# Kernel tuning notes

Hardware: AMD Instinct MI355X
Metric: run time of the kernel (lower is better)

The kernel has to match this reference:

```python
import jax, jax.numpy as jnp
import numpy as np

B, N, M, D = 128, 256, 8, 768  # batch, input patches, memory tokens, embed dim


def setup_inputs() -> dict:
    key = jax.random.key(0)
    ks = jax.random.split(key, 6)
    w_scale = D ** -0.5
    return {
        "x": jax.random.normal(ks[0], (B, N, D), dtype=jnp.float32),
        "memory": jax.random.normal(ks[1], (M, D), dtype=jnp.float32) * 0.02,
        "Wq": jax.random.normal(ks[2], (D, D), dtype=jnp.float32) * w_scale,
        "bq": jnp.zeros((D,), dtype=jnp.float32),
        "Wk": jax.random.normal(ks[3], (D, D), dtype=jnp.float32) * w_scale,
        "bk": jnp.zeros((D,), dtype=jnp.float32),
        "Wv": jax.random.normal(ks[4], (D, D), dtype=jnp.float32) * w_scale,
        "bv": jnp.zeros((D,), dtype=jnp.float32),
        "Wo": jax.random.normal(ks[5], (D, D), dtype=jnp.float32) * w_scale,
        "bo": jnp.zeros((D,), dtype=jnp.float32),
    }


def reference(x, memory, Wq, bq, Wk, bk, Wv, bv, Wo, bo):
    b, n, d = x.shape
    m = memory.shape[0]
    t = n + m
    scaling = d ** -0.5  # mha.scaling = 1/sqrt(input_dim)
    # concat input patches with expanded memory tokens: [B, T, D]
    cat = jnp.concatenate([x, jnp.broadcast_to(memory[None], (b, m, d))], axis=1)
    q = cat @ Wq + bq
    k = cat @ Wk + bk
    v = cat @ Wv + bv
    # full attention matrix [B, T, T], softmax over keys
    att = jax.nn.softmax(jnp.einsum("bqd,bkd->bqk", q, k) * scaling, axis=-1)
    # post-softmax multiplicative mask: zero all rows for memory-token queries
    row_mask = (jnp.arange(t) < n).astype(att.dtype)[None, :, None]  # [1, T, 1]
    att = att * row_mask
    head_out = jnp.einsum("bqk,bkd->bqd", att, v)
    attended = head_out @ Wo + bo
    # return only the input-patch part (split(...)[0])
    return attended[:, :n, :]
```

## Files before the change

kernel.cpp:

```cpp
#include <hip/hip_runtime.h>
#include <hip/hip_bf16.h>

typedef __attribute__((ext_vector_type(4))) float f32x4;
typedef __attribute__((ext_vector_type(8))) short short8;
typedef __attribute__((ext_vector_type(4))) unsigned short us4;
typedef unsigned short u16;

#define DEVI __device__ __forceinline__

#define BB 128
#define NN 256
#define MMEM 8
#define DD 768
#define TT 264
#define TP 320
#define SP 384
#define AROWS2 33024

DEVI u16 f2bf(float f) {
  __hip_bfloat16 b = __float2bfloat16(f);
  u16 u; __builtin_memcpy(&u, &b, 2); return u;
}

DEVI void gload_lds16(const void* g, void* l) {
  __builtin_amdgcn_global_load_lds((const __attribute__((address_space(1))) void*)g,
                                   (__attribute__((address_space(3))) void*)l, 16, 0, 0);
}


__global__ __launch_bounds__(256)
void conv_x(const float* __restrict__ x, const float* __restrict__ mem, u16* __restrict__ Ab) {
  const long total4 = (long)AROWS2 * DD / 4;
  for (long i = (long)blockIdx.x * blockDim.x + threadIdx.x; i < total4;
       i += (long)gridDim.x * blockDim.x) {
    long e = i * 4;
    int row = (int)(e / DD);
    int cb  = (int)(e % DD);
    f32x4 v = {0.f, 0.f, 0.f, 0.f};
    if (row < BB * NN)             v = *(const f32x4*)(x   + (size_t)row * DD + cb);
    else if (row < BB * NN + MMEM) v = *(const f32x4*)(mem + (size_t)(row - BB * NN) * DD + cb);
    us4 o = {f2bf(v[0]), f2bf(v[1]), f2bf(v[2]), f2bf(v[3])};
    *(us4*)(Ab + e) = o;
  }
}

__global__ __launch_bounds__(256)
void conv_w(const float* __restrict__ Wq, const float* __restrict__ Wk,
            const float* __restrict__ Wv, const float* __restrict__ Wo,
            u16* __restrict__ Wqt, u16* __restrict__ Wkt,
            u16* __restrict__ Wvt, u16* __restrict__ Wot) {
  const int total = 4 * DD * DD;
  for (int i = blockIdx.x * blockDim.x + threadIdx.x; i < total;
       i += gridDim.x * blockDim.x) {
    int mat = i / (DD * DD), rem = i % (DD * DD);
    int j = rem / DD, d = rem % DD;
    const float* W = (mat == 0) ? Wq : (mat == 1) ? Wk : (mat == 2) ? Wv : Wo;
    u16* Wt = (mat == 0) ? Wqt : (mat == 1) ? Wkt : (mat == 2) ? Wvt : Wot;
    Wt[(size_t)j * DD + d] = f2bf(W[(size_t)d * DD + j]);
  }
}


#define BAR()    __builtin_amdgcn_s_barrier()
#define CFENCE() asm volatile("" ::: "memory")
#define VMW8()   asm volatile("s_waitcnt vmcnt(8)" ::: "memory")

#define STG(gb, isB, ss, rg, kt) do {                                          \
    const u16* _s = (gb) + (size_t)((rg) * 16 + srow) * DD + (kt) * 64 + scol; \
    char* _d = smem + (ss) * 65536 + (isB) * 32768 + (rg) * 2048;              \
    gload_lds16(_s, _d);                                                       \
    gload_lds16(_s + 32, _d + 1024);                                           \
  } while (0)

#define STG_A0(ss, kt) STG(Ab, 0, ss, ((w & 3) | ((w & 4) << 1)), kt)
#define STG_B0(ss, kt) STG(Bb, 1, ss, ((w & 1) | ((w & 6) << 1)), kt)
#define STG_A1(ss, kt) STG(Ab, 0, ss, (((w & 3) | ((w & 4) << 1)) + 4), kt)
#define STG_B1(ss, kt) STG(Bb, 1, ss, (((w & 1) | ((w & 6) << 1)) + 2), kt)

#define RD_A(dst, s, QM)                                                          \
  _Pragma("unroll") for (int mi = 0; mi < 4; ++mi)                                \
  _Pragma("unroll") for (int ks = 0; ks < 2; ++ks)                                \
    dst[mi][ks] = *(const short8*)(smem + (s) * 65536 +                           \
                    ((wm * 8 + (QM) * 4 + mi) * 2 + ks) * 1024 + fbase);

#define RD_B(dst, s, QN)                                                          \
  _Pragma("unroll") for (int ni = 0; ni < 2; ++ni)                                \
  _Pragma("unroll") for (int ks = 0; ks < 2; ++ks)                                \
    dst[ni][ks] = *(const short8*)(smem + (s) * 65536 + 32768 +                   \
                    ((wn * 4 + (QN) * 2 + ni) * 2 + ks) * 1024 + fbase);

#define MM(FA, FB, QM, QN)                                                        \
  _Pragma("unroll") for (int mi = 0; mi < 4; ++mi)                                \
  _Pragma("unroll") for (int ni = 0; ni < 2; ++ni)                                \
  _Pragma("unroll") for (int ks = 0; ks < 2; ++ks)                                \
    acc[(QM)*4+mi][(QN)*2+ni] = __builtin_amdgcn_mfma_f32_16x16x32_bf16(          \
        FA[mi][ks], FB[ni][ks], acc[(QM)*4+mi][(QN)*2+ni], 0, 0, 0);

template<int MODE>
__global__ __launch_bounds__(512)
void gemm256(const u16* __restrict__ A, const u16* __restrict__ Bq,
             const u16* __restrict__ Bk, const u16* __restrict__ Bv,
             const float* __restrict__ b0, const float* __restrict__ b1,
             const float* __restrict__ b2,
             u16* __restrict__ Oq, u16* __restrict__ Ok, u16* __restrict__ Ov,
             float* __restrict__ FO, int NT)
{
  extern __shared__ char smem[];
  const int tid = threadIdx.x;
  const int l = tid & 63;
  const int w = tid >> 6;
  const int wm = w >> 2, wn = w & 3;

  const int nwg = gridDim.x * gridDim.y;
  const int lin = blockIdx.y * gridDim.x + blockIdx.x;
  const int qq = nwg >> 3, rr = nwg & 7;
  const int xcd = lin & 7, idx = lin >> 3;
  const int wg = (xcd < rr ? xcd * (qq + 1) : rr * (qq + 1) + (xcd - rr) * qq) + idx;
  const int tn = wg % gridDim.x, tm = wg / gridDim.x;

  const u16* Ab = A + (size_t)tm * 256 * DD;
  const u16* Bb;
  int matsel = 0;
  if constexpr (MODE == 0) {
    matsel = tn / 3;
    const u16* Wp = (matsel == 0) ? Bq : (matsel == 1) ? Bk : Bv;
    Bb = Wp + (size_t)(tn % 3) * 256 * DD;
  } else {
    Bb = Bq + (size_t)tn * 256 * DD;
  }

  const int jj = (l < 32) ? l : (l ^ 2);
  const int srow = jj >> 2;
  const int scol = (jj & 3) * 8;
  const int fbase = (((l & 15) * 64) + ((l >> 4) * 16)) ^ (((l >> 3) & 1) << 5);

  f32x4 acc[8][4];
  #pragma unroll
  for (int i = 0; i < 8; ++i)
    #pragma unroll
    for (int jx = 0; jx < 4; ++jx) acc[i][jx] = (f32x4){0.f, 0.f, 0.f, 0.f};

  short8 fa0[4][2], fa1[4][2], fb0[2][2], fb1[2][2];

  STG_A0(0, 0); STG_B0(0, 0); STG_A1(0, 0); STG_B1(0, 0);

  for (int g = 0; g < NT; ++g) {
    const int s = g & 1, ss = s ^ 1;
    const int st = (g + 1 < NT) ? (g + 1) : 0;

    CFENCE(); BAR(); CFENCE();
    STG_A0(ss, st); STG_B0(ss, st); STG_A1(ss, st); STG_B1(ss, st);
    VMW8();
    BAR(); CFENCE();

    RD_A(fa0, s, 0); RD_B(fb0, s, 0);
    __builtin_amdgcn_s_setprio(1); MM(fa0, fb0, 0, 0); __builtin_amdgcn_s_setprio(0);
    RD_A(fa1, s, 1);
    __builtin_amdgcn_s_setprio(1); MM(fa1, fb0, 1, 0); __builtin_amdgcn_s_setprio(0);
    RD_B(fb1, s, 1);
    __builtin_amdgcn_s_setprio(1); MM(fa1, fb1, 1, 1); MM(fa0, fb1, 0, 1);
    __builtin_amdgcn_s_setprio(0);
  }

  const int fr = l & 15, fro = (l >> 4) * 4;
  if constexpr (MODE == 0) {
    const float* bias = (matsel == 0) ? b0 : (matsel == 1) ? b1 : b2;
    u16* ob = (matsel == 0) ? Oq : (matsel == 1) ? Ok : Ov;
    const int cb = (tn % 3) * 256 + wn * 64;
    const size_t rb = (size_t)tm * 256 + wm * 128;
    #pragma unroll
    for (int MI = 0; MI < 8; ++MI)
      #pragma unroll
      for (int NI = 0; NI < 4; ++NI) {
        const int col = cb + NI * 16 + fr;
        const float bvv = bias[col];
        #pragma unroll
        for (int r = 0; r < 4; ++r)
          ob[(rb + MI * 16 + fro + r) * DD + col] = f2bf(acc[MI][NI][r] + bvv);
      }
  } else {
    const int cb = tn * 256 + wn * 64;
    const size_t rb = (size_t)tm * 256 + wm * 128;
    #pragma unroll
    for (int MI = 0; MI < 8; ++MI)
      #pragma unroll
      for (int NI = 0; NI < 4; ++NI) {
        const int col = cb + NI * 16 + fr;
        const float bvv = b0[col];
        #pragma unroll
        for (int r = 0; r < 4; ++r)
          FO[(rb + MI * 16 + fro + r) * DD + col] = acc[MI][NI][r] + bvv;
      }
  }
}


template<int MODE>
__global__ __launch_bounds__(256)
void gemm_bt(const u16* __restrict__ A, const u16* __restrict__ Bm,
             const float* __restrict__ f0,
             u16* __restrict__ U0, float* __restrict__ F0, int Kdim)
{
  const int tid = threadIdx.x;
  const int l  = tid & 63;
  const int w  = tid >> 6;
  const int wm = w >> 1, wn = w & 1;
  const int tm = blockIdx.x, tn = blockIdx.y, z = blockIdx.z;

  __shared__ u16 lsA[128 * 32];
  __shared__ u16 lsB[128 * 32];

  const u16* Abase; int lda;
  if constexpr (MODE == 1)      { Abase = A + ((size_t)z * NN + tm * 128) * DD; lda = DD; }
  else                          { Abase = A + ((size_t)z * NN + tm * 128) * TP; lda = TP; }

  const u16* Bbase; int ldb;
  if constexpr (MODE == 1) { Bbase = Bm; ldb = DD; }
  else                     { Bbase = Bm + ((size_t)z * DD + tn * 128) * TP; ldb = TP; }

  f32x4 acc[4][4];
  #pragma unroll
  for (int i = 0; i < 4; i++)
    #pragma unroll
    for (int j = 0; j < 4; j++) acc[i][j] = (f32x4){0.f, 0.f, 0.f, 0.f};

  const int srow = l >> 2;
  const int scol = (l & 3) * 8;
  const int nkt = Kdim >> 5;

  for (int kt = 0; kt < nkt; ++kt) {
    const int kpos = kt * 32 + scol;
    #pragma unroll
    for (int q = 0; q < 2; ++q) {
      const int r = q * 64 + w * 16 + srow;
      gload_lds16(Abase + (size_t)r * lda + kpos, &lsA[q * 2048 + w * 512]);
    }
    #pragma unroll
    for (int q = 0; q < 2; ++q) {
      const int r = q * 64 + w * 16 + srow;
      const u16* src;
      if constexpr (MODE == 1) {
        const int t = tn * 128 + r;
        const int rr = (t < NN) ? (z * NN + t)
                     : ((t < TT) ? (BB * NN + t - NN) : BB * NN);
        src = Bm + (size_t)rr * DD + kpos;
      } else {
        src = Bbase + (size_t)r * ldb + kpos;
      }
      gload_lds16(src, &lsB[q * 2048 + w * 512]);
    }
    __syncthreads();

    const int fr = l & 15, fk = (l >> 4) * 8;
    short8 fa[4], fb[4];
    #pragma unroll
    for (int mi = 0; mi < 4; mi++)
      fa[mi] = *(const short8*)&lsA[(wm * 64 + mi * 16 + fr) * 32 + fk];
    #pragma unroll
    for (int ni = 0; ni < 4; ni++)
      fb[ni] = *(const short8*)&lsB[(wn * 64 + ni * 16 + fr) * 32 + fk];
    #pragma unroll
    for (int mi = 0; mi < 4; mi++)
      #pragma unroll
      for (int ni = 0; ni < 4; ni++)
        acc[mi][ni] = __builtin_amdgcn_mfma_f32_16x16x32_bf16(fa[mi], fb[ni], acc[mi][ni], 0, 0, 0);
    __syncthreads();
  }

  const int fr  = l & 15;
  const int fro = (l >> 4) * 4;

  if constexpr (MODE == 1) {
    const float scl = 0.03608439182435161f;
    float* Sb = F0 + (size_t)z * NN * SP;
    const int cb = tn * 128 + wn * 64;
    const int rb = tm * 128 + wm * 64;
    #pragma unroll
    for (int mi = 0; mi < 4; mi++)
      #pragma unroll
      for (int ni = 0; ni < 4; ni++)
        #pragma unroll
        for (int r = 0; r < 4; r++)
          Sb[(size_t)(rb + mi * 16 + fro + r) * SP + cb + ni * 16 + fr] = acc[mi][ni][r] * scl;
  } else {
    const int cb = tn * 128 + wn * 64;
    const size_t rb = (size_t)z * NN + tm * 128 + wm * 64;
    #pragma unroll
    for (int mi = 0; mi < 4; mi++)
      #pragma unroll
      for (int ni = 0; ni < 4; ni++)
        #pragma unroll
        for (int r = 0; r < 4; r++)
          U0[(rb + mi * 16 + fro + r) * DD + cb + ni * 16 + fr] = f2bf(acc[mi][ni][r]);
  }
}


__global__ __launch_bounds__(256)
void softmax_k(const float* __restrict__ S, u16* __restrict__ P) {
  const int l = threadIdx.x & 63;
  const int row = blockIdx.x * 4 + (threadIdx.x >> 6);
  const float* s = S + (size_t)row * SP;
  float v0 = s[l], v1 = s[64 + l], v2 = s[128 + l], v3 = s[192 + l];
  float v4 = (l < 8) ? s[256 + l] : -__builtin_inff();
  float m = fmaxf(fmaxf(fmaxf(v0, v1), fmaxf(v2, v3)), v4);
  #pragma unroll
  for (int off = 32; off; off >>= 1) m = fmaxf(m, __shfl_xor(m, off));
  float e0 = __expf(v0 - m), e1 = __expf(v1 - m), e2 = __expf(v2 - m), e3 = __expf(v3 - m);
  float e4 = (l < 8) ? __expf(v4 - m) : 0.f;
  float sum = e0 + e1 + e2 + e3 + e4;
  #pragma unroll
  for (int off = 32; off; off >>= 1) sum += __shfl_xor(sum, off);
  const float inv = 1.f / sum;
  u16* p = P + (size_t)row * TP;
  p[l] = f2bf(e0 * inv); p[64 + l] = f2bf(e1 * inv);
  p[128 + l] = f2bf(e2 * inv); p[192 + l] = f2bf(e3 * inv);
  if (l < 8) p[256 + l] = f2bf(e4 * inv);
  else       p[256 + l] = 0;
}


__global__ __launch_bounds__(256)
void transpose_v(const u16* __restrict__ V, u16* __restrict__ Vt) {
  __shared__ u16 ls[64 * 66];
  const int b = blockIdx.z;
  const int d0 = blockIdx.x * 64;
  const int t0 = blockIdx.y * 64;
  const int tid = threadIdx.x;
  #pragma unroll
  for (int q = 0; q < 2; ++q) {
    const int idx = q * 256 + tid;
    const int tr = idx >> 3;
    const int dg = (idx & 7) * 8;
    const int t = t0 + tr;
    short8 v = (short8)(short)0;
    if (t < NN)       v = *(const short8*)(V + ((size_t)b * NN + t) * DD + d0 + dg);
    else if (t < TT)  v = *(const short8*)(V + (size_t)(BB * NN + t - NN) * DD + d0 + dg);
    #pragma unroll
    for (int e = 0; e < 8; ++e) ls[tr * 66 + dg + e] = (u16)v[e];
  }
  __syncthreads();
  #pragma unroll
  for (int q = 0; q < 2; ++q) {
    const int idx = q * 256 + tid;
    const int dr = idx >> 3;
    const int tg = (idx & 7) * 8;
    short8 v;
    #pragma unroll
    for (int e = 0; e < 8; ++e) v[e] = (short)ls[(tg + e) * 66 + dr];
    *(short8*)(Vt + ((size_t)b * DD + d0 + dr) * TP + t0 + tg) = v;
  }
}


extern "C" void kernel_launch(void* const* d_in, const int* in_sizes, int n_in,
                              void* d_out, int out_size, void* d_ws, size_t ws_size,
                              hipStream_t stream) {
  const float* x   = (const float*)d_in[0];
  const float* mem = (const float*)d_in[1];
  const float* Wq  = (const float*)d_in[2];
  const float* bq  = (const float*)d_in[3];
  const float* Wk  = (const float*)d_in[4];
  const float* bk  = (const float*)d_in[5];
  const float* Wv  = (const float*)d_in[6];
  const float* bv  = (const float*)d_in[7];
  const float* Wo  = (const float*)d_in[8];
  const float* bo  = (const float*)d_in[9];
  float* out = (float*)d_out;
  (void)ws_size; (void)in_sizes; (void)n_in; (void)out_size;

  const size_t QKV_B = (size_t)AROWS2 * DD * 2;
  char* wsb = (char*)d_ws;
  u16* Qb  = (u16*)(wsb);
  u16* Kb  = (u16*)(wsb + QKV_B);
  u16* Vb  = (u16*)(wsb + 2 * QKV_B);
  u16* Vt  = (u16*)(wsb);
  u16* O   = (u16*)(wsb + (size_t)BB * DD * TP * 2);
  u16* Wot = (u16*)(wsb + 3 * QKV_B);

  u16*   Ab  = (u16*)d_out;
  float* S   = (float*)d_out;
  u16*   P   = (u16*)((char*)d_out + QKV_B);
  u16*   Wqt = (u16*)((char*)d_out + 97124352);
  u16*   Wkt = Wqt + (size_t)DD * DD;
  u16*   Wvt = Wkt + (size_t)DD * DD;

  conv_x<<<2048, 256, 0, stream>>>(x, mem, Ab);
  conv_w<<<1024, 256, 0, stream>>>(Wq, Wk, Wv, Wo, Wqt, Wkt, Wvt, Wot);

  gemm256<0><<<dim3(9, 129), 512, 131072, stream>>>(
      Ab, Wqt, Wkt, Wvt, bq, bk, bv, Qb, Kb, Vb, nullptr, DD / 64);

  gemm_bt<1><<<dim3(2, 3, BB), 256, 0, stream>>>(Qb, Kb, nullptr, nullptr, S, DD);

  softmax_k<<<8192, 256, 0, stream>>>(S, P);

  transpose_v<<<dim3(12, 5, BB), 256, 0, stream>>>(Vb, Vt);

  gemm_bt<2><<<dim3(2, 6, BB), 256, 0, stream>>>(P, Vt, nullptr, O, nullptr, TP);

  gemm256<1><<<dim3(3, 128), 512, 131072, stream>>>(
      O, Wot, nullptr, nullptr, bo, nullptr, nullptr,
      nullptr, nullptr, nullptr, out, DD / 64);
}
```

Before: 361.3 us.

## Interleave LDS staging with MFMA in gemm256 and route P@V through it

Restructures the gemm256 main loop so global-to-LDS loads for the next k-tile are issued in four pieces between MFMA groups, with partial vmcnt waits and barriers. Fragments for the next stage are prefetched at the end of each iteration. This replaces the single bulk-stage-then-wait pattern. The P@V batched GEMM moves from the small 128x128 gemm_bt kernel to a new gemm256 mode with 256x256 tiles and a K of 320 (five k-tiles). The goals are better load/compute overlap and more data reuse in the attention-value product. The cost is more barriers per iteration, and the new synchronisation needs careful correctness checks.

```diff
diff --git a/kernel.cpp b/kernel.cpp
--- a/kernel.cpp
+++ b/kernel.cpp
@@ -63,19 +63,20 @@
 
 #define BAR()    __builtin_amdgcn_s_barrier()
 #define CFENCE() asm volatile("" ::: "memory")
-#define VMW8()   asm volatile("s_waitcnt vmcnt(8)" ::: "memory")
-
-#define STG(gb, isB, ss, rg, kt) do {                                          \
-    const u16* _s = (gb) + (size_t)((rg) * 16 + srow) * DD + (kt) * 64 + scol; \
-    char* _d = smem + (ss) * 65536 + (isB) * 32768 + (rg) * 2048;              \
-    gload_lds16(_s, _d);                                                       \
-    gload_lds16(_s + 32, _d + 1024);                                           \
+#define VM2()    asm volatile("s_waitcnt vmcnt(2)" ::: "memory")
+#define VMW0()   asm volatile("s_waitcnt vmcnt(0)" ::: "memory")
+
+#define STG(gb, ld, isB, ss, rg, kt) do {                                       \
+    const u16* _s = (gb) + (size_t)((rg) * 16 + srow) * (ld) + (kt) * 64 + scol;\
+    char* _d = smem + (ss) * 65536 + (isB) * 32768 + (rg) * 2048;               \
+    gload_lds16(_s, _d);                                                        \
+    gload_lds16(_s + 32, _d + 1024);                                            \
   } while (0)
 
-#define STG_A0(ss, kt) STG(Ab, 0, ss, ((w & 3) | ((w & 4) << 1)), kt)
-#define STG_B0(ss, kt) STG(Bb, 1, ss, ((w & 1) | ((w & 6) << 1)), kt)
-#define STG_A1(ss, kt) STG(Ab, 0, ss, (((w & 3) | ((w & 4) << 1)) + 4), kt)
-#define STG_B1(ss, kt) STG(Bb, 1, ss, (((w & 1) | ((w & 6) << 1)) + 2), kt)
+#define STG_A0(ss, kt) STG(Ab, LDA, 0, ss, ((w & 3) | ((w & 4) << 1)), kt)
+#define STG_B0(ss, kt) STG(Bb, LDB, 1, ss, ((w & 1) | ((w & 6) << 1)), kt)
+#define STG_A1(ss, kt) STG(Ab, LDA, 0, ss, (((w & 3) | ((w & 4) << 1)) + 4), kt)
+#define STG_B1(ss, kt) STG(Bb, LDB, 1, ss, (((w & 1) | ((w & 6) << 1)) + 2), kt)
 
 #define RD_A(dst, s, QM)                                                          \
   _Pragma("unroll") for (int mi = 0; mi < 4; ++mi)                                \
@@ -111,22 +112,30 @@
   const int w = tid >> 6;
   const int wm = w >> 2, wn = w & 3;
 
+  constexpr int LDA = (MODE == 2) ? TP : DD;
+  constexpr int LDB = (MODE == 2) ? TP : DD;
+
   const int nwg = gridDim.x * gridDim.y;
   const int lin = blockIdx.y * gridDim.x + blockIdx.x;
   const int qq = nwg >> 3, rr = nwg & 7;
   const int xcd = lin & 7, idx = lin >> 3;
   const int wg = (xcd < rr ? xcd * (qq + 1) : rr * (qq + 1) + (xcd - rr) * qq) + idx;
-  const int tn = wg % gridDim.x, tm = wg / gridDim.x;
-
-  const u16* Ab = A + (size_t)tm * 256 * DD;
-  const u16* Bb;
+  const int tn = wg % gridDim.x;
+  const int tmz = wg / gridDim.x;
+
+  const u16* Ab; const u16* Bb;
   int matsel = 0;
   if constexpr (MODE == 0) {
+    Ab = A + (size_t)tmz * 256 * DD;
     matsel = tn / 3;
     const u16* Wp = (matsel == 0) ? Bq : (matsel == 1) ? Bk : Bv;
     Bb = Wp + (size_t)(tn % 3) * 256 * DD;
+  } else if constexpr (MODE == 1) {
+    Ab = A + (size_t)tmz * 256 * DD;
+    Bb = Bq + (size_t)tn * 256 * DD;
   } else {
-    Bb = Bq + (size_t)tn * 256 * DD;
+    Ab = A + (size_t)tmz * NN * TP;
+    Bb = Bq + ((size_t)tmz * DD + tn * 256) * TP;
   }
 
   const int jj = (l < 32) ? l : (l ^ 2);
@@ -143,23 +152,30 @@
   short8 fa0[4][2], fa1[4][2], fb0[2][2], fb1[2][2];
 
   STG_A0(0, 0); STG_B0(0, 0); STG_A1(0, 0); STG_B1(0, 0);
+  VMW0(); BAR(); CFENCE();
+  RD_A(fa0, 0, 0); RD_B(fb0, 0, 0);
 
   for (int g = 0; g < NT; ++g) {
     const int s = g & 1, ss = s ^ 1;
-    const int st = (g + 1 < NT) ? (g + 1) : 0;
-
-    CFENCE(); BAR(); CFENCE();
-    STG_A0(ss, st); STG_B0(ss, st); STG_A1(ss, st); STG_B1(ss, st);
-    VMW8();
-    BAR(); CFENCE();
-
-    RD_A(fa0, s, 0); RD_B(fb0, s, 0);
+    const int st = (g + 1 < NT) ? (g + 1) : (NT - 1);
+
+    VM2(); BAR(); CFENCE();
+    RD_A(fa1, s, 1);
+    STG_A0(ss, st);
     __builtin_amdgcn_s_setprio(1); MM(fa0, fb0, 0, 0); __builtin_amdgcn_s_setprio(0);
-    RD_A(fa1, s, 1);
+
+    VM2(); BAR(); CFENCE();
+    RD_B(fb1, s, 1);
+    STG_B0(ss, st);
     __builtin_amdgcn_s_setprio(1); MM(fa1, fb0, 1, 0); __builtin_amdgcn_s_setprio(0);
-    RD_B(fb1, s, 1);
-    __builtin_amdgcn_s_setprio(1); MM(fa1, fb1, 1, 1); MM(fa0, fb1, 0, 1);
-    __builtin_amdgcn_s_setprio(0);
+
+    STG_A1(ss, st);
+    __builtin_amdgcn_s_setprio(1); MM(fa0, fb1, 0, 1); __builtin_amdgcn_s_setprio(0);
+
+    VM2(); BAR(); CFENCE();
+    RD_A(fa0, ss, 0); RD_B(fb0, ss, 0);
+    STG_B1(ss, st);
+    __builtin_amdgcn_s_setprio(1); MM(fa1, fb1, 1, 1); __builtin_amdgcn_s_setprio(0);
   }
 
   const int fr = l & 15, fro = (l >> 4) * 4;
@@ -167,7 +183,7 @@
     const float* bias = (matsel == 0) ? b0 : (matsel == 1) ? b1 : b2;
     u16* ob = (matsel == 0) ? Oq : (matsel == 1) ? Ok : Ov;
     const int cb = (tn % 3) * 256 + wn * 64;
-    const size_t rb = (size_t)tm * 256 + wm * 128;
+    const size_t rb = (size_t)tmz * 256 + wm * 128;
     #pragma unroll
     for (int MI = 0; MI < 8; ++MI)
       #pragma unroll
@@ -178,9 +194,9 @@
         for (int r = 0; r < 4; ++r)
           ob[(rb + MI * 16 + fro + r) * DD + col] = f2bf(acc[MI][NI][r] + bvv);
       }
-  } else {
+  } else if constexpr (MODE == 1) {
     const int cb = tn * 256 + wn * 64;
-    const size_t rb = (size_t)tm * 256 + wm * 128;
+    const size_t rb = (size_t)tmz * 256 + wm * 128;
     #pragma unroll
     for (int MI = 0; MI < 8; ++MI)
       #pragma unroll
@@ -191,15 +207,25 @@
         for (int r = 0; r < 4; ++r)
           FO[(rb + MI * 16 + fro + r) * DD + col] = acc[MI][NI][r] + bvv;
       }
-  }
-}
-
-
-template<int MODE>
+  } else {
+    const int cb = tn * 256 + wn * 64;
+    const size_t rb = (size_t)tmz * NN + wm * 128;
+    #pragma unroll
+    for (int MI = 0; MI < 8; ++MI)
+      #pragma unroll
+      for (int NI = 0; NI < 4; ++NI) {
+        const int col = cb + NI * 16 + fr;
+        #pragma unroll
+        for (int r = 0; r < 4; ++r)
+          Oq[(rb + MI * 16 + fro + r) * DD + col] = f2bf(acc[MI][NI][r]);
+      }
+  }
+}
+
+
 __global__ __launch_bounds__(256)
-void gemm_bt(const u16* __restrict__ A, const u16* __restrict__ Bm,
-             const float* __restrict__ f0,
-             u16* __restrict__ U0, float* __restrict__ F0, int Kdim)
+void gemm_s(const u16* __restrict__ A, const u16* __restrict__ Bm,
+            float* __restrict__ F0)
 {
   const int tid = threadIdx.x;
   const int l  = tid & 63;
@@ -210,13 +236,7 @@
   __shared__ u16 lsA[128 * 32];
   __shared__ u16 lsB[128 * 32];
 
-  const u16* Abase; int lda;
-  if constexpr (MODE == 1)      { Abase = A + ((size_t)z * NN + tm * 128) * DD; lda = DD; }
-  else                          { Abase = A + ((size_t)z * NN + tm * 128) * TP; lda = TP; }
-
-  const u16* Bbase; int ldb;
-  if constexpr (MODE == 1) { Bbase = Bm; ldb = DD; }
-  else                     { Bbase = Bm + ((size_t)z * DD + tn * 128) * TP; ldb = TP; }
+  const u16* Abase = A + ((size_t)z * NN + tm * 128) * DD;
 
   f32x4 acc[4][4];
   #pragma unroll
@@ -226,28 +246,21 @@
 
   const int srow = l >> 2;
   const int scol = (l & 3) * 8;
-  const int nkt = Kdim >> 5;
-
-  for (int kt = 0; kt < nkt; ++kt) {
+
+  for (int kt = 0; kt < 24; ++kt) {
     const int kpos = kt * 32 + scol;
     #pragma unroll
     for (int q = 0; q < 2; ++q) {
       const int r = q * 64 + w * 16 + srow;
-      gload_lds16(Abase + (size_t)r * lda + kpos, &lsA[q * 2048 + w * 512]);
+      gload_lds16(Abase + (size_t)r * DD + kpos, &lsA[q * 2048 + w * 512]);
     }
     #pragma unroll
     for (int q = 0; q < 2; ++q) {
       const int r = q * 64 + w * 16 + srow;
-      const u16* src;
-      if constexpr (MODE == 1) {
-        const int t = tn * 128 + r;
-        const int rr = (t < NN) ? (z * NN + t)
-                     : ((t < TT) ? (BB * NN + t - NN) : BB * NN);
-        src = Bm + (size_t)rr * DD + kpos;
-      } else {
-        src = Bbase + (size_t)r * ldb + kpos;
-      }
-      gload_lds16(src, &lsB[q * 2048 + w * 512]);
+      const int t = tn * 128 + r;
+      const int rr = (t < NN) ? (z * NN + t)
+                   : ((t < TT) ? (BB * NN + t - NN) : BB * NN);
+      gload_lds16(Bm + (size_t)rr * DD + kpos, &lsB[q * 2048 + w * 512]);
     }
     __syncthreads();
 
@@ -269,30 +282,17 @@
 
   const int fr  = l & 15;
   const int fro = (l >> 4) * 4;
-
-  if constexpr (MODE == 1) {
-    const float scl = 0.03608439182435161f;
-    float* Sb = F0 + (size_t)z * NN * SP;
-    const int cb = tn * 128 + wn * 64;
-    const int rb = tm * 128 + wm * 64;
-    #pragma unroll
-    for (int mi = 0; mi < 4; mi++)
+  const float scl = 0.03608439182435161f;
+  float* Sb = F0 + (size_t)z * NN * SP;
+  const int cb = tn * 128 + wn * 64;
+  const int rb = tm * 128 + wm * 64;
+  #pragma unroll
+  for (int mi = 0; mi < 4; mi++)
+    #pragma unroll
+    for (int ni = 0; ni < 4; ni++)
       #pragma unroll
-      for (int ni = 0; ni < 4; ni++)
-        #pragma unroll
-        for (int r = 0; r < 4; r++)
-          Sb[(size_t)(rb + mi * 16 + fro + r) * SP + cb + ni * 16 + fr] = acc[mi][ni][r] * scl;
-  } else {
-    const int cb = tn * 128 + wn * 64;
-    const size_t rb = (size_t)z * NN + tm * 128 + wm * 64;
-    #pragma unroll
-    for (int mi = 0; mi < 4; mi++)
-      #pragma unroll
-      for (int ni = 0; ni < 4; ni++)
-        #pragma unroll
-        for (int r = 0; r < 4; r++)
-          U0[(rb + mi * 16 + fro + r) * DD + cb + ni * 16 + fr] = f2bf(acc[mi][ni][r]);
-  }
+      for (int r = 0; r < 4; r++)
+        Sb[(size_t)(rb + mi * 16 + fro + r) * SP + cb + ni * 16 + fr] = acc[mi][ni][r] * scl;
 }
 
 
@@ -389,17 +389,19 @@
   conv_w<<<1024, 256, 0, stream>>>(Wq, Wk, Wv, Wo, Wqt, Wkt, Wvt, Wot);
 
   gemm256<0><<<dim3(9, 129), 512, 131072, stream>>>(
-      Ab, Wqt, Wkt, Wvt, bq, bk, bv, Qb, Kb, Vb, nullptr, DD / 64);
-
-  gemm_bt<1><<<dim3(2, 3, BB), 256, 0, stream>>>(Qb, Kb, nullptr, nullptr, S, DD);
+      Ab, Wqt, Wkt, Wvt, bq, bk, bv, Qb, Kb, Vb, nullptr, 12);
+
+  gemm_s<<<dim3(2, 3, BB), 256, 0, stream>>>(Qb, Kb, S);
 
   softmax_k<<<8192, 256, 0, stream>>>(S, P);
 
   transpose_v<<<dim3(12, 5, BB), 256, 0, stream>>>(Vb, Vt);
 
-  gemm_bt<2><<<dim3(2, 6, BB), 256, 0, stream>>>(P, Vt, nullptr, O, nullptr, TP);
+  gemm256<2><<<dim3(3, 128), 512, 131072, stream>>>(
+      P, Vt, nullptr, nullptr, nullptr, nullptr, nullptr,
+      O, nullptr, nullptr, nullptr, 5);
 
   gemm256<1><<<dim3(3, 128), 512, 131072, stream>>>(
       O, Wot, nullptr, nullptr, bo, nullptr, nullptr,
-      nullptr, nullptr, nullptr, out, DD / 64);
-}
+      nullptr, nullptr, nullptr, out, 12);
+}
```

After: 333.0 us. -7.8%, faster.
